# Kernel optimization log

Measured on AMD Instinct MI355X. Metric: run time of the kernel, lower is better.

Reference implementation:

```python
import jax, jax.numpy as jnp
import numpy as np

N = 100000      # num nodes
C = 48          # feature / label dim
E = 1600000     # num edges (avg in-degree 16)
M = 20000       # num labeled nodes
L = 10          # diffusion_layer
LAM = 0.9       # lambda_


def setup_inputs() -> dict:
    key = jax.random.key(0)
    k1, k2, k3, k4, k5 = jax.random.split(key, 5)
    Z = jax.random.normal(k1, (N, C), dtype=jnp.float32)
    Y = jax.random.uniform(k2, (M, C), dtype=jnp.float32)
    mask = jax.random.randint(k3, (M,), 0, N, dtype=jnp.int32)
    # ensure every node has in-degree >= 1 so deg**-0.5 stays finite
    row = jax.random.randint(k4, (E,), 0, N, dtype=jnp.int32)
    col = jnp.concatenate([jnp.arange(N, dtype=jnp.int32),
                           jax.random.randint(k5, (E - N,), 0, N, dtype=jnp.int32)])
    edge_index = jnp.stack([row, col])  # [2, E]
    return {"Z": Z, "Y": Y, "mask": mask, "edge_index": edge_index, "beta": 0}


def reference(Z, Y, mask, edge_index, beta):
    num_nodes = Z.shape[0]
    # G = Z.clone(); G[mask] = Y   (noise=False branch is identity)
    G = Z.at[mask].set(Y)
    row, col = edge_index[0], edge_index[1]
    # degree_vector = sparse.sum(adj, 0)  -> column sums (in-degree), duplicates accumulate
    deg = jax.ops.segment_sum(jnp.ones(col.shape, Z.dtype), col, num_segments=num_nodes)
    dinv = deg ** -0.5
    # normalized edge weights of D^{-1/2} A D^{-1/2}
    w = dinv[row] * dinv[col]  # [E]

    def step(x, _):
        # x <- lambda * (adj @ x) + (1 - lambda) * G
        agg = jax.ops.segment_sum(w[:, None] * x[col], row, num_segments=num_nodes)
        return agg * LAM + (1.0 - LAM) * G, None

    x, _ = jax.lax.scan(step, G, None, length=L)
    return x
```

## Files before the change

### kernel.cpp

```cpp
#include <hip/hip_runtime.h>
#include <hip/hip_fp16.h>

#define FEAT 48
#define CH 12
#define STEPS 10
#define BK 256
#define NBMAX 512
#define CAP 5120
constexpr float LAM   = 0.9f;
constexpr float OMLAM = 0.1f;


__global__ void setup_kernel(int* __restrict__ bcur, int* __restrict__ ccur, int nb,
                             const int* __restrict__ mask, int* __restrict__ winner, int M) {
    int i = blockIdx.x * blockDim.x + threadIdx.x;
    if (i < nb) { bcur[i] = i * CAP; ccur[i] = i * CAP; }
    if (i < M) atomicMax(&winner[mask[i]], i);
}

__global__ __launch_bounds__(1024)
void bucket_scatter(const int* __restrict__ row, const int* __restrict__ col,
                    int* __restrict__ bcur, int* __restrict__ ccur,
                    unsigned int* __restrict__ bstore, unsigned char* __restrict__ cstore,
                    int E, int nb, int nblk) {
    __shared__ int hr[NBMAX], cr[NBMAX], hc[NBMAX], cc[NBMAX];
    int tid = threadIdx.x;
    int ce = (E + nblk - 1) / nblk;
    int s = blockIdx.x * ce;
    int e_end = min(E, s + ce);
    for (int i = tid; i < nb; i += blockDim.x) { hr[i] = 0; hc[i] = 0; }
    __syncthreads();
    for (int i = s + tid; i < e_end; i += blockDim.x) {
        atomicAdd(&hr[row[i] >> 8], 1);
        atomicAdd(&hc[col[i] >> 8], 1);
    }
    __syncthreads();
    for (int i = tid; i < nb; i += blockDim.x) {
        cr[i] = hr[i] ? atomicAdd(&bcur[i], hr[i]) : 0;
        cc[i] = hc[i] ? atomicAdd(&ccur[i], hc[i]) : 0;
    }
    __syncthreads();
    for (int i = s + tid; i < e_end; i += blockDim.x) {
        int r = row[i], c = col[i];
        int pr = atomicAdd(&cr[r >> 8], 1);
        bstore[pr] = ((unsigned int)c << 8) | (unsigned int)(r & (BK - 1));
        int pc = atomicAdd(&cc[c >> 8], 1);
        cstore[pc] = (unsigned char)(c & (BK - 1));
    }
}

__global__ void bucket_prefix(const int* __restrict__ bcur, int* __restrict__ bpre,
                              int* __restrict__ off, int nb, int E, int N) {
    __shared__ int sh[NBMAX];
    int tid = threadIdx.x;
    int tot = (tid < nb) ? (bcur[tid] - tid * CAP) : 0;
    sh[tid] = tot;
    __syncthreads();
    for (int d = 1; d < NBMAX; d <<= 1) {
        int v = (tid >= d) ? sh[tid - d] : 0;
        __syncthreads();
        sh[tid] += v;
        __syncthreads();
    }
    if (tid < nb) bpre[tid] = sh[tid] - tot;
    if (tid == 0) off[N] = E;
}

__global__ void finish_kernel(const unsigned int* __restrict__ bstore,
                              const int* __restrict__ bcur, const int* __restrict__ bpre,
                              const unsigned char* __restrict__ cstore,
                              const int* __restrict__ ccur,
                              int* __restrict__ off, int* __restrict__ csr_col,
                              float* __restrict__ dinv, int N) {
    __shared__ int h[BK], loc[BK], cur[BK];
    int b = blockIdx.x, tid = threadIdx.x;
    int cnt  = bcur[b] - b * CAP;
    int base = bpre[b];
    const unsigned int* src = bstore + (size_t)b * CAP;
    h[tid] = 0;
    __syncthreads();
    for (int i = tid; i < cnt; i += BK) atomicAdd(&h[src[i] & (BK - 1)], 1);
    __syncthreads();
    int v = h[tid];
    loc[tid] = v;
    __syncthreads();
    for (int d = 1; d < BK; d <<= 1) {
        int t = (tid >= d) ? loc[tid - d] : 0;
        __syncthreads();
        loc[tid] += t;
        __syncthreads();
    }
    int excl = loc[tid] - v;
    int r = b * BK + tid;
    if (r < N) off[r] = base + excl;
    cur[tid] = excl;
    __syncthreads();
    for (int i = tid; i < cnt; i += BK) {
        unsigned int e = src[i];
        int p = atomicAdd(&cur[e & (BK - 1)], 1);
        csr_col[base + p] = (int)(e >> 8);
    }
    __syncthreads();
    h[tid] = 0;
    __syncthreads();
    int ccnt = ccur[b] - b * CAP;
    const unsigned char* csrc = cstore + (size_t)b * CAP;
    for (int i = tid; i < ccnt; i += BK) atomicAdd(&h[csrc[i]], 1);
    __syncthreads();
    int c = b * BK + tid;
    if (c < N) dinv[c] = (float)(1.0 / sqrt((double)h[tid]));
}

__global__ void prep_kernel(const float4* __restrict__ Z4, const float4* __restrict__ Y4,
                            const int* __restrict__ winner, const float* __restrict__ dinv,
                            float4* __restrict__ G4, uint2* __restrict__ u0, int N) {
    int t = blockIdx.x * blockDim.x + threadIdx.x;
    if (t >= N * CH) return;
    int r = t / CH, q = t - r * CH;
    int w = winner[r];
    float4 g = (w >= 0) ? Y4[(size_t)w * CH + q] : Z4[t];
    G4[t] = g;
    float d = dinv[r];
    __half2 h0 = __floats2half2_rn(d * g.x, d * g.y);
    __half2 h1 = __floats2half2_rn(d * g.z, d * g.w);
    u0[t] = make_uint2(__builtin_bit_cast(unsigned int, h0),
                       __builtin_bit_cast(unsigned int, h1));
}

#define ACC4(v)                                                                      \
    do {                                                                             \
        float2 f_;                                                                   \
        f_ = __half22float2(__builtin_bit_cast(__half2, (v).x)); ax += f_.x; ay += f_.y; \
        f_ = __half22float2(__builtin_bit_cast(__half2, (v).y)); az += f_.x; aw += f_.y; \
    } while (0)

template<bool LAST>
__global__ void diffuse_kernel(const uint2* __restrict__ up, const uint2* __restrict__ u0,
                               const float* __restrict__ dinv, const float4* __restrict__ G4,
                               const int* __restrict__ off, const int* __restrict__ cols,
                               uint2* __restrict__ uout, float4* __restrict__ xout, int N) {
    int t = blockIdx.x * blockDim.x + threadIdx.x;
    if (t >= N * CH) return;
    int r = t / CH, q = t - r * CH;
    int j0 = off[r], j1 = off[r + 1];
    float ax = 0.f, ay = 0.f, az = 0.f, aw = 0.f;

    int j = j0;
    for (; j + 8 <= j1; j += 8) {
        int c0 = cols[j],     c1 = cols[j + 1], c2 = cols[j + 2], c3 = cols[j + 3];
        int c4 = cols[j + 4], c5 = cols[j + 5], c6 = cols[j + 6], c7 = cols[j + 7];
        uint2 v0 = up[(size_t)c0 * CH + q];
        uint2 v1 = up[(size_t)c1 * CH + q];
        uint2 v2 = up[(size_t)c2 * CH + q];
        uint2 v3 = up[(size_t)c3 * CH + q];
        uint2 v4 = up[(size_t)c4 * CH + q];
        uint2 v5 = up[(size_t)c5 * CH + q];
        uint2 v6 = up[(size_t)c6 * CH + q];
        uint2 v7 = up[(size_t)c7 * CH + q];
        ACC4(v0); ACC4(v1); ACC4(v2); ACC4(v3);
        ACC4(v4); ACC4(v5); ACC4(v6); ACC4(v7);
    }
    if (j + 4 <= j1) {
        int c0 = cols[j], c1 = cols[j + 1], c2 = cols[j + 2], c3 = cols[j + 3];
        uint2 v0 = up[(size_t)c0 * CH + q];
        uint2 v1 = up[(size_t)c1 * CH + q];
        uint2 v2 = up[(size_t)c2 * CH + q];
        uint2 v3 = up[(size_t)c3 * CH + q];
        ACC4(v0); ACC4(v1); ACC4(v2); ACC4(v3);
        j += 4;
    }
    if (j < j1) {
        int c0 = cols[j];
        int c1 = (j + 1 < j1) ? cols[j + 1] : c0;
        int c2 = (j + 2 < j1) ? cols[j + 2] : c0;
        uint2 v0 = up[(size_t)c0 * CH + q];
        uint2 v1 = up[(size_t)c1 * CH + q];
        uint2 v2 = up[(size_t)c2 * CH + q];
        ACC4(v0);
        if (j + 1 < j1) ACC4(v1);
        if (j + 2 < j1) ACC4(v2);
    }

    float d = dinv[r];
    if (LAST) {
        float4 g = G4[t];
        float4 o;
        float s = LAM * d;
        o.x = fmaf(s, ax, OMLAM * g.x);
        o.y = fmaf(s, ay, OMLAM * g.y);
        o.z = fmaf(s, az, OMLAM * g.z);
        o.w = fmaf(s, aw, OMLAM * g.w);
        xout[t] = o;
    } else {
        float a = LAM * d * d;
        uint2 z = u0[t];
        float2 b0 = __half22float2(__builtin_bit_cast(__half2, z.x));
        float2 b1 = __half22float2(__builtin_bit_cast(__half2, z.y));
        __half2 h0 = __floats2half2_rn(fmaf(a, ax, OMLAM * b0.x),
                                       fmaf(a, ay, OMLAM * b0.y));
        __half2 h1 = __floats2half2_rn(fmaf(a, az, OMLAM * b1.x),
                                       fmaf(a, aw, OMLAM * b1.y));
        uout[t] = make_uint2(__builtin_bit_cast(unsigned int, h0),
                             __builtin_bit_cast(unsigned int, h1));
    }
}


extern "C" void kernel_launch(void* const* d_in, const int* in_sizes, int n_in,
                              void* d_out, int out_size, void* d_ws, size_t ws_size,
                              hipStream_t stream) {
    const float* Z    = (const float*)d_in[0];
    const float* Y    = (const float*)d_in[1];
    const int*   mask = (const int*)d_in[2];
    const int*   ei   = (const int*)d_in[3];

    const int N = in_sizes[0] / FEAT;
    const int M = in_sizes[2];
    const int E = in_sizes[3] / 2;
    const int* row = ei;
    const int* col = ei + E;
    const int NB = (N + BK - 1) / BK;

    char* ws = (char*)d_ws;
    size_t pos = 0;
    auto alloc = [&](size_t bytes) -> void* {
        void* p = ws + pos;
        pos = (pos + bytes + 255) & ~(size_t)255;
        return p;
    };
    float* G      = (float*)alloc((size_t)N * FEAT * 4);
    uint2* u0     = (uint2*)alloc((size_t)N * CH * 8);
    uint2* ua     = (uint2*)alloc((size_t)N * CH * 8);
    uint2* ub     = (uint2*)alloc((size_t)N * CH * 8);
    float* dinv   = (float*)alloc((size_t)N * 4);
    int*   off    = (int*)  alloc((size_t)(N + 1) * 4);
    int*   winner = (int*)  alloc((size_t)N * 4);
    int*   csr    = (int*)  alloc((size_t)E * 4);
    unsigned int*  bstore = (unsigned int*) alloc((size_t)NB * CAP * 4);
    unsigned char* cstore = (unsigned char*)alloc((size_t)NB * CAP);
    int*   bcur   = (int*)  alloc((size_t)NBMAX * 4);
    int*   ccur   = (int*)  alloc((size_t)NBMAX * 4);
    int*   bpre   = (int*)  alloc((size_t)NBMAX * 4);

    hipMemsetAsync(winner, 0xFF, (size_t)N * 4, stream);

    const int B = 256;
    const int setup_n = max(NB, M);
    setup_kernel<<<(setup_n + B - 1) / B, B, 0, stream>>>(bcur, ccur, NB, mask, winner, M);

    const int SBLK = 256;
    bucket_scatter<<<SBLK, 1024, 0, stream>>>(row, col, bcur, ccur, bstore, cstore, E, NB, SBLK);
    bucket_prefix <<<1, NBMAX, 0, stream>>>(bcur, bpre, off, NB, E, N);
    finish_kernel <<<NB, BK, 0, stream>>>(bstore, bcur, bpre, cstore, ccur,
                                          off, csr, dinv, N);

    prep_kernel<<<(N * CH + B - 1) / B, B, 0, stream>>>((const float4*)Z, (const float4*)Y,
                                                        winner, dinv, (float4*)G, u0, N);

    const int nt = N * CH;
    const uint2* src = u0;
    uint2* bufs[2] = { ua, ub };
    for (int it = 0; it < STEPS - 1; ++it) {
        uint2* dst = bufs[it & 1];
        diffuse_kernel<false><<<(nt + B - 1) / B, B, 0, stream>>>(
            src, u0, dinv, (const float4*)G, off, csr, dst, nullptr, N);
        src = dst;
    }
    diffuse_kernel<true><<<(nt + B - 1) / B, B, 0, stream>>>(
        src, u0, dinv, (const float4*)G, off, csr, nullptr, (float4*)d_out, N);
}
```

Measured before the change: 421.3 us.

## Renumber nodes by row degree to balance warps in diffusion SpMM

Adds a counting sort of rows by out-degree, building a permutation, a permuted CSR with remapped column indices, and permuted dinv and offsets. Diffusion then runs in permuted order, so rows of similar degree share a wavefront, which reduces divergence from uneven neighbor counts. The final step scatters results back through the permutation. The main gather loop drops from 8-way to 4-way unrolling. The cost is extra setup kernels and memory, and the renumbering may scatter neighbor locality in the gathered feature reads.

```diff
diff --git a/kernel.cpp b/kernel.cpp
--- a/kernel.cpp
+++ b/kernel.cpp
@@ -7,6 +7,7 @@
 #define BK 256
 #define NBMAX 512
 #define CAP 5120
+#define DB 512
 constexpr float LAM   = 0.9f;
 constexpr float OMLAM = 0.1f;
 
@@ -71,7 +72,7 @@
                               const unsigned char* __restrict__ cstore,
                               const int* __restrict__ ccur,
                               int* __restrict__ off, int* __restrict__ csr_col,
-                              float* __restrict__ dinv, int N) {
+                              float* __restrict__ dinv, int* __restrict__ rowdeg, int N) {
     __shared__ int h[BK], loc[BK], cur[BK];
     int b = blockIdx.x, tid = threadIdx.x;
     int cnt  = bcur[b] - b * CAP;
@@ -92,7 +93,7 @@
     }
     int excl = loc[tid] - v;
     int r = b * BK + tid;
-    if (r < N) off[r] = base + excl;
+    if (r < N) { off[r] = base + excl; rowdeg[r] = v; }
     cur[tid] = excl;
     __syncthreads();
     for (int i = tid; i < cnt; i += BK) {
@@ -111,16 +112,96 @@
     if (c < N) dinv[c] = (float)(1.0 / sqrt((double)h[tid]));
 }
 
+
+__global__ void sort_hist(const int* __restrict__ rowdeg, int* __restrict__ dbin,
+                          int N, int nblk) {
+    __shared__ int h[DB];
+    int tid = threadIdx.x;
+    for (int i = tid; i < DB; i += blockDim.x) h[i] = 0;
+    __syncthreads();
+    int ce = (N + nblk - 1) / nblk;
+    int s = blockIdx.x * ce, e = min(N, s + ce);
+    for (int i = s + tid; i < e; i += blockDim.x)
+        atomicAdd(&h[min(rowdeg[i], DB - 1)], 1);
+    __syncthreads();
+    for (int i = tid; i < DB; i += blockDim.x)
+        if (h[i]) atomicAdd(&dbin[i], h[i]);
+}
+
+__global__ void sort_scan(const int* __restrict__ dbin, int* __restrict__ rbase,
+                          int* __restrict__ ebase, int* __restrict__ dcur) {
+    __shared__ int s1[DB], s2[DB];
+    int tid = threadIdx.x;
+    int c = dbin[tid];
+    s1[tid] = c;
+    s2[tid] = c * tid;
+    __syncthreads();
+    for (int d = 1; d < DB; d <<= 1) {
+        int v1 = (tid >= d) ? s1[tid - d] : 0;
+        int v2 = (tid >= d) ? s2[tid - d] : 0;
+        __syncthreads();
+        s1[tid] += v1; s2[tid] += v2;
+        __syncthreads();
+    }
+    rbase[tid] = s1[tid] - c;
+    ebase[tid] = s2[tid] - c * tid;
+    dcur[tid]  = s1[tid] - c;
+}
+
+__global__ void sort_scatter(const int* __restrict__ rowdeg, const float* __restrict__ dinv,
+                             int* __restrict__ dcur, const int* __restrict__ rbase,
+                             const int* __restrict__ ebase,
+                             int* __restrict__ perm, int* __restrict__ perm_inv,
+                             int* __restrict__ off2, float* __restrict__ dinv2,
+                             int N, int E, int nblk) {
+    __shared__ int h[DB], cur[DB];
+    int tid = threadIdx.x;
+    for (int i = tid; i < DB; i += blockDim.x) h[i] = 0;
+    __syncthreads();
+    int ce = (N + nblk - 1) / nblk;
+    int s = blockIdx.x * ce, e = min(N, s + ce);
+    for (int i = s + tid; i < e; i += blockDim.x)
+        atomicAdd(&h[min(rowdeg[i], DB - 1)], 1);
+    __syncthreads();
+    for (int i = tid; i < DB; i += blockDim.x)
+        cur[i] = h[i] ? atomicAdd(&dcur[i], h[i]) : 0;
+    __syncthreads();
+    for (int i = s + tid; i < e; i += blockDim.x) {
+        int deg = rowdeg[i];
+        int b = min(deg, DB - 1);
+        int pos = atomicAdd(&cur[b], 1);
+        perm[pos] = i;
+        perm_inv[i] = pos;
+        off2[pos] = ebase[b] + (pos - rbase[b]) * deg;
+        dinv2[pos] = dinv[i];
+    }
+    if (blockIdx.x == 0 && tid == 0) off2[N] = E;
+}
+
+__global__ void remap_kernel(const int* __restrict__ perm, const int* __restrict__ perm_inv,
+                             const int* __restrict__ off, const int* __restrict__ off2,
+                             const int* __restrict__ csr, int* __restrict__ csr2, int N) {
+    int i = blockIdx.x * blockDim.x + threadIdx.x;
+    if (i >= N) return;
+    int r = perm[i];
+    int sb = off[r], j0 = off2[i];
+    int deg = off2[i + 1] - j0;
+    for (int k = 0; k < deg; ++k)
+        csr2[j0 + k] = perm_inv[csr[sb + k]];
+}
+
 __global__ void prep_kernel(const float4* __restrict__ Z4, const float4* __restrict__ Y4,
-                            const int* __restrict__ winner, const float* __restrict__ dinv,
+                            const int* __restrict__ winner, const float* __restrict__ dinv2,
+                            const int* __restrict__ perm,
                             float4* __restrict__ G4, uint2* __restrict__ u0, int N) {
     int t = blockIdx.x * blockDim.x + threadIdx.x;
     if (t >= N * CH) return;
-    int r = t / CH, q = t - r * CH;
+    int i = t / CH, q = t - i * CH;
+    int r = perm[i];
     int w = winner[r];
-    float4 g = (w >= 0) ? Y4[(size_t)w * CH + q] : Z4[t];
+    float4 g = (w >= 0) ? Y4[(size_t)w * CH + q] : Z4[(size_t)r * CH + q];
     G4[t] = g;
-    float d = dinv[r];
+    float d = dinv2[i];
     __half2 h0 = __floats2half2_rn(d * g.x, d * g.y);
     __half2 h1 = __floats2half2_rn(d * g.z, d * g.w);
     u0[t] = make_uint2(__builtin_bit_cast(unsigned int, h0),
@@ -136,38 +217,24 @@
 
 template<bool LAST>
 __global__ void diffuse_kernel(const uint2* __restrict__ up, const uint2* __restrict__ u0,
-                               const float* __restrict__ dinv, const float4* __restrict__ G4,
-                               const int* __restrict__ off, const int* __restrict__ cols,
+                               const float* __restrict__ dinv2, const float4* __restrict__ G4,
+                               const int* __restrict__ off2, const int* __restrict__ cols,
+                               const int* __restrict__ perm,
                                uint2* __restrict__ uout, float4* __restrict__ xout, int N) {
     int t = blockIdx.x * blockDim.x + threadIdx.x;
     if (t >= N * CH) return;
-    int r = t / CH, q = t - r * CH;
-    int j0 = off[r], j1 = off[r + 1];
+    int i = t / CH, q = t - i * CH;
+    int j0 = off2[i], j1 = off2[i + 1];
     float ax = 0.f, ay = 0.f, az = 0.f, aw = 0.f;
 
     int j = j0;
-    for (; j + 8 <= j1; j += 8) {
-        int c0 = cols[j],     c1 = cols[j + 1], c2 = cols[j + 2], c3 = cols[j + 3];
-        int c4 = cols[j + 4], c5 = cols[j + 5], c6 = cols[j + 6], c7 = cols[j + 7];
-        uint2 v0 = up[(size_t)c0 * CH + q];
-        uint2 v1 = up[(size_t)c1 * CH + q];
-        uint2 v2 = up[(size_t)c2 * CH + q];
-        uint2 v3 = up[(size_t)c3 * CH + q];
-        uint2 v4 = up[(size_t)c4 * CH + q];
-        uint2 v5 = up[(size_t)c5 * CH + q];
-        uint2 v6 = up[(size_t)c6 * CH + q];
-        uint2 v7 = up[(size_t)c7 * CH + q];
-        ACC4(v0); ACC4(v1); ACC4(v2); ACC4(v3);
-        ACC4(v4); ACC4(v5); ACC4(v6); ACC4(v7);
-    }
-    if (j + 4 <= j1) {
+    for (; j + 4 <= j1; j += 4) {
         int c0 = cols[j], c1 = cols[j + 1], c2 = cols[j + 2], c3 = cols[j + 3];
         uint2 v0 = up[(size_t)c0 * CH + q];
         uint2 v1 = up[(size_t)c1 * CH + q];
         uint2 v2 = up[(size_t)c2 * CH + q];
         uint2 v3 = up[(size_t)c3 * CH + q];
         ACC4(v0); ACC4(v1); ACC4(v2); ACC4(v3);
-        j += 4;
     }
     if (j < j1) {
         int c0 = cols[j];
@@ -181,7 +248,7 @@
         if (j + 2 < j1) ACC4(v2);
     }
 
-    float d = dinv[r];
+    float d = dinv2[i];
     if (LAST) {
         float4 g = G4[t];
         float4 o;
@@ -190,7 +257,7 @@
         o.y = fmaf(s, ay, OMLAM * g.y);
         o.z = fmaf(s, az, OMLAM * g.z);
         o.w = fmaf(s, aw, OMLAM * g.w);
-        xout[t] = o;
+        xout[(size_t)perm[i] * CH + q] = o;
     } else {
         float a = LAM * d * d;
         uint2 z = u0[t];
@@ -233,16 +300,27 @@
     uint2* ua     = (uint2*)alloc((size_t)N * CH * 8);
     uint2* ub     = (uint2*)alloc((size_t)N * CH * 8);
     float* dinv   = (float*)alloc((size_t)N * 4);
+    float* dinv2  = (float*)alloc((size_t)N * 4);
     int*   off    = (int*)  alloc((size_t)(N + 1) * 4);
+    int*   off2   = (int*)  alloc((size_t)(N + 1) * 4);
     int*   winner = (int*)  alloc((size_t)N * 4);
+    int*   rowdeg = (int*)  alloc((size_t)N * 4);
+    int*   perm   = (int*)  alloc((size_t)N * 4);
+    int*   pinv   = (int*)  alloc((size_t)N * 4);
     int*   csr    = (int*)  alloc((size_t)E * 4);
+    int*   csr2   = (int*)  alloc((size_t)E * 4);
     unsigned int*  bstore = (unsigned int*) alloc((size_t)NB * CAP * 4);
     unsigned char* cstore = (unsigned char*)alloc((size_t)NB * CAP);
     int*   bcur   = (int*)  alloc((size_t)NBMAX * 4);
     int*   ccur   = (int*)  alloc((size_t)NBMAX * 4);
     int*   bpre   = (int*)  alloc((size_t)NBMAX * 4);
+    int*   dbin   = (int*)  alloc((size_t)DB * 4);
+    int*   rbase  = (int*)  alloc((size_t)DB * 4);
+    int*   ebase  = (int*)  alloc((size_t)DB * 4);
+    int*   dcur   = (int*)  alloc((size_t)DB * 4);
 
     hipMemsetAsync(winner, 0xFF, (size_t)N * 4, stream);
+    hipMemsetAsync(dbin,   0,    (size_t)DB * 4, stream);
 
     const int B = 256;
     const int setup_n = max(NB, M);
@@ -252,10 +330,17 @@
     bucket_scatter<<<SBLK, 1024, 0, stream>>>(row, col, bcur, ccur, bstore, cstore, E, NB, SBLK);
     bucket_prefix <<<1, NBMAX, 0, stream>>>(bcur, bpre, off, NB, E, N);
     finish_kernel <<<NB, BK, 0, stream>>>(bstore, bcur, bpre, cstore, ccur,
-                                          off, csr, dinv, N);
+                                          off, csr, dinv, rowdeg, N);
+
+    const int HBLK = 128;
+    sort_hist   <<<HBLK, 256, 0, stream>>>(rowdeg, dbin, N, HBLK);
+    sort_scan   <<<1, DB, 0, stream>>>(dbin, rbase, ebase, dcur);
+    sort_scatter<<<HBLK, 256, 0, stream>>>(rowdeg, dinv, dcur, rbase, ebase,
+                                           perm, pinv, off2, dinv2, N, E, HBLK);
+    remap_kernel<<<(N + B - 1) / B, B, 0, stream>>>(perm, pinv, off, off2, csr, csr2, N);
 
     prep_kernel<<<(N * CH + B - 1) / B, B, 0, stream>>>((const float4*)Z, (const float4*)Y,
-                                                        winner, dinv, (float4*)G, u0, N);
+                                                        winner, dinv2, perm, (float4*)G, u0, N);
 
     const int nt = N * CH;
     const uint2* src = u0;
@@ -263,9 +348,9 @@
     for (int it = 0; it < STEPS - 1; ++it) {
         uint2* dst = bufs[it & 1];
         diffuse_kernel<false><<<(nt + B - 1) / B, B, 0, stream>>>(
-            src, u0, dinv, (const float4*)G, off, csr, dst, nullptr, N);
+            src, u0, dinv2, (const float4*)G, off2, csr2, perm, dst, nullptr, N);
         src = dst;
     }
     diffuse_kernel<true><<<(nt + B - 1) / B, B, 0, stream>>>(
-        src, u0, dinv, (const float4*)G, off, csr, nullptr, (float4*)d_out, N);
-}
+        src, u0, dinv2, (const float4*)G, off2, csr2, perm, nullptr, (float4*)d_out, N);
+}
```

Result: slower. 465.7 us (+10.5%).

## Split feature diffusion into separate 8-chunk and 4-chunk channel slabs

Applied to the files above, without the earlier changes.

Splits the half-precision feature state into two separately stored slabs: one with 32 channels (64-byte rows) and one with 16 channels (32-byte rows). Each slab runs its own full 10-step diffusion chain. The aim is a smaller gathered working set per pass and row strides aligned to cache lines, so neighbor gathers should hit cache more often. In exchange, the CSR offsets and column indices are read twice per step and the number of kernel launches doubles.

```diff
diff --git a/kernel.cpp b/kernel.cpp
--- a/kernel.cpp
+++ b/kernel.cpp
@@ -3,6 +3,8 @@
 
 #define FEAT 48
 #define CH 12
+#define CHA 8
+#define CHB 4
 #define STEPS 10
 #define BK 256
 #define NBMAX 512
@@ -113,7 +115,8 @@
 
 __global__ void prep_kernel(const float4* __restrict__ Z4, const float4* __restrict__ Y4,
                             const int* __restrict__ winner, const float* __restrict__ dinv,
-                            float4* __restrict__ G4, uint2* __restrict__ u0, int N) {
+                            float4* __restrict__ G4,
+                            uint2* __restrict__ u0a, uint2* __restrict__ u0b, int N) {
     int t = blockIdx.x * blockDim.x + threadIdx.x;
     if (t >= N * CH) return;
     int r = t / CH, q = t - r * CH;
@@ -123,8 +126,10 @@
     float d = dinv[r];
     __half2 h0 = __floats2half2_rn(d * g.x, d * g.y);
     __half2 h1 = __floats2half2_rn(d * g.z, d * g.w);
-    u0[t] = make_uint2(__builtin_bit_cast(unsigned int, h0),
-                       __builtin_bit_cast(unsigned int, h1));
+    uint2 val = make_uint2(__builtin_bit_cast(unsigned int, h0),
+                           __builtin_bit_cast(unsigned int, h1));
+    if (q < CHA) u0a[(size_t)r * CHA + q]         = val;
+    else         u0b[(size_t)r * CHB + (q - CHA)] = val;
 }
 
 #define ACC4(v)                                                                      \
@@ -134,14 +139,14 @@
         f_ = __half22float2(__builtin_bit_cast(__half2, (v).y)); az += f_.x; aw += f_.y; \
     } while (0)
 
-template<bool LAST>
+template<int CHP, int FOFF, bool LAST>
 __global__ void diffuse_kernel(const uint2* __restrict__ up, const uint2* __restrict__ u0,
                                const float* __restrict__ dinv, const float4* __restrict__ G4,
                                const int* __restrict__ off, const int* __restrict__ cols,
                                uint2* __restrict__ uout, float4* __restrict__ xout, int N) {
     int t = blockIdx.x * blockDim.x + threadIdx.x;
-    if (t >= N * CH) return;
-    int r = t / CH, q = t - r * CH;
+    if (t >= N * CHP) return;
+    int r = t / CHP, q = t - r * CHP;
     int j0 = off[r], j1 = off[r + 1];
     float ax = 0.f, ay = 0.f, az = 0.f, aw = 0.f;
 
@@ -149,23 +154,23 @@
     for (; j + 8 <= j1; j += 8) {
         int c0 = cols[j],     c1 = cols[j + 1], c2 = cols[j + 2], c3 = cols[j + 3];
         int c4 = cols[j + 4], c5 = cols[j + 5], c6 = cols[j + 6], c7 = cols[j + 7];
-        uint2 v0 = up[(size_t)c0 * CH + q];
-        uint2 v1 = up[(size_t)c1 * CH + q];
-        uint2 v2 = up[(size_t)c2 * CH + q];
-        uint2 v3 = up[(size_t)c3 * CH + q];
-        uint2 v4 = up[(size_t)c4 * CH + q];
-        uint2 v5 = up[(size_t)c5 * CH + q];
-        uint2 v6 = up[(size_t)c6 * CH + q];
-        uint2 v7 = up[(size_t)c7 * CH + q];
+        uint2 v0 = up[(size_t)c0 * CHP + q];
+        uint2 v1 = up[(size_t)c1 * CHP + q];
+        uint2 v2 = up[(size_t)c2 * CHP + q];
+        uint2 v3 = up[(size_t)c3 * CHP + q];
+        uint2 v4 = up[(size_t)c4 * CHP + q];
+        uint2 v5 = up[(size_t)c5 * CHP + q];
+        uint2 v6 = up[(size_t)c6 * CHP + q];
+        uint2 v7 = up[(size_t)c7 * CHP + q];
         ACC4(v0); ACC4(v1); ACC4(v2); ACC4(v3);
         ACC4(v4); ACC4(v5); ACC4(v6); ACC4(v7);
     }
     if (j + 4 <= j1) {
         int c0 = cols[j], c1 = cols[j + 1], c2 = cols[j + 2], c3 = cols[j + 3];
-        uint2 v0 = up[(size_t)c0 * CH + q];
-        uint2 v1 = up[(size_t)c1 * CH + q];
-        uint2 v2 = up[(size_t)c2 * CH + q];
-        uint2 v3 = up[(size_t)c3 * CH + q];
+        uint2 v0 = up[(size_t)c0 * CHP + q];
+        uint2 v1 = up[(size_t)c1 * CHP + q];
+        uint2 v2 = up[(size_t)c2 * CHP + q];
+        uint2 v3 = up[(size_t)c3 * CHP + q];
         ACC4(v0); ACC4(v1); ACC4(v2); ACC4(v3);
         j += 4;
     }
@@ -173,9 +178,9 @@
         int c0 = cols[j];
         int c1 = (j + 1 < j1) ? cols[j + 1] : c0;
         int c2 = (j + 2 < j1) ? cols[j + 2] : c0;
-        uint2 v0 = up[(size_t)c0 * CH + q];
-        uint2 v1 = up[(size_t)c1 * CH + q];
-        uint2 v2 = up[(size_t)c2 * CH + q];
+        uint2 v0 = up[(size_t)c0 * CHP + q];
+        uint2 v1 = up[(size_t)c1 * CHP + q];
+        uint2 v2 = up[(size_t)c2 * CHP + q];
         ACC4(v0);
         if (j + 1 < j1) ACC4(v1);
         if (j + 2 < j1) ACC4(v2);
@@ -183,14 +188,14 @@
 
     float d = dinv[r];
     if (LAST) {
-        float4 g = G4[t];
+        float4 g = G4[(size_t)r * CH + FOFF + q];
         float4 o;
         float s = LAM * d;
         o.x = fmaf(s, ax, OMLAM * g.x);
         o.y = fmaf(s, ay, OMLAM * g.y);
         o.z = fmaf(s, az, OMLAM * g.z);
         o.w = fmaf(s, aw, OMLAM * g.w);
-        xout[t] = o;
+        xout[(size_t)r * CH + FOFF + q] = o;
     } else {
         float a = LAM * d * d;
         uint2 z = u0[t];
@@ -229,9 +234,12 @@
         return p;
     };
     float* G      = (float*)alloc((size_t)N * FEAT * 4);
-    uint2* u0     = (uint2*)alloc((size_t)N * CH * 8);
-    uint2* ua     = (uint2*)alloc((size_t)N * CH * 8);
-    uint2* ub     = (uint2*)alloc((size_t)N * CH * 8);
+    uint2* ua0    = (uint2*)alloc((size_t)N * CHA * 8);
+    uint2* uaa    = (uint2*)alloc((size_t)N * CHA * 8);
+    uint2* uab    = (uint2*)alloc((size_t)N * CHA * 8);
+    uint2* ub0    = (uint2*)alloc((size_t)N * CHB * 8);
+    uint2* uba    = (uint2*)alloc((size_t)N * CHB * 8);
+    uint2* ubb    = (uint2*)alloc((size_t)N * CHB * 8);
     float* dinv   = (float*)alloc((size_t)N * 4);
     int*   off    = (int*)  alloc((size_t)(N + 1) * 4);
     int*   winner = (int*)  alloc((size_t)N * 4);
@@ -255,17 +263,32 @@
                                           off, csr, dinv, N);
 
     prep_kernel<<<(N * CH + B - 1) / B, B, 0, stream>>>((const float4*)Z, (const float4*)Y,
-                                                        winner, dinv, (float4*)G, u0, N);
-
-    const int nt = N * CH;
-    const uint2* src = u0;
-    uint2* bufs[2] = { ua, ub };
-    for (int it = 0; it < STEPS - 1; ++it) {
-        uint2* dst = bufs[it & 1];
-        diffuse_kernel<false><<<(nt + B - 1) / B, B, 0, stream>>>(
-            src, u0, dinv, (const float4*)G, off, csr, dst, nullptr, N);
-        src = dst;
-    }
-    diffuse_kernel<true><<<(nt + B - 1) / B, B, 0, stream>>>(
-        src, u0, dinv, (const float4*)G, off, csr, nullptr, (float4*)d_out, N);
-}
+                                                        winner, dinv, (float4*)G, ua0, ub0, N);
+
+    {
+        const int nt = N * CHA;
+        const uint2* src = ua0;
+        uint2* bufs[2] = { uaa, uab };
+        for (int it = 0; it < STEPS - 1; ++it) {
+            uint2* dst = bufs[it & 1];
+            diffuse_kernel<CHA, 0, false><<<(nt + B - 1) / B, B, 0, stream>>>(
+                src, ua0, dinv, (const float4*)G, off, csr, dst, nullptr, N);
+            src = dst;
+        }
+        diffuse_kernel<CHA, 0, true><<<(nt + B - 1) / B, B, 0, stream>>>(
+            src, ua0, dinv, (const float4*)G, off, csr, nullptr, (float4*)d_out, N);
+    }
+    {
+        const int nt = N * CHB;
+        const uint2* src = ub0;
+        uint2* bufs[2] = { uba, ubb };
+        for (int it = 0; it < STEPS - 1; ++it) {
+            uint2* dst = bufs[it & 1];
+            diffuse_kernel<CHB, CHA, false><<<(nt + B - 1) / B, B, 0, stream>>>(
+                src, ub0, dinv, (const float4*)G, off, csr, dst, nullptr, N);
+            src = dst;
+        }
+        diffuse_kernel<CHB, CHA, true><<<(nt + B - 1) / B, B, 0, stream>>>(
+            src, ub0, dinv, (const float4*)G, off, csr, nullptr, (float4*)d_out, N);
+    }
+}
```

New measurement: 447.7 us. +6.3%, slower.
